# Kernel optimization log

Measured on AMD Instinct MI355X. Metric: run time of the kernel, lower is better.

Reference implementation:

```python
import jax, jax.numpy as jnp
import numpy as np

N_ENTITIES = 100_000
N_USERS = 50_000
N_HOPS = 3
R0, R1 = 42033, 44630  # hard-coded region slice in the source (2597 regions)
CHANNEL = 128
N_EDGES = 2_000_000
NNZ = 1_000_000
N_REL_ROWS = 25  # n_relations - 1


def setup_inputs() -> dict:
    key = jax.random.key(0)
    ks = jax.random.split(key, 10)
    user_emb = jax.random.normal(ks[0], (N_USERS, CHANNEL), jnp.float32) * 0.1
    entity_emb = jax.random.normal(ks[1], (N_ENTITIES, CHANNEL), jnp.float32) * 0.1
    edge_head = jax.random.randint(ks[2], (N_EDGES,), 0, N_ENTITIES, dtype=jnp.int32)
    edge_tail = jax.random.randint(ks[3], (N_EDGES,), 0, N_ENTITIES, dtype=jnp.int32)
    # edge_type in [1, n_relations-1] because weight is indexed with edge_type - 1
    edge_type = jax.random.randint(ks[4], (N_EDGES,), 1, N_REL_ROWS + 1, dtype=jnp.int32)
    interact_rows = jax.random.randint(ks[5], (NNZ,), 0, N_USERS, dtype=jnp.int32)
    interact_cols = jax.random.randint(ks[6], (NNZ,), 0, N_ENTITIES, dtype=jnp.int32)
    interact_vals = jax.random.uniform(ks[7], (NNZ,), jnp.float32)
    rw = jax.random.uniform(ks[8], (R1 - R0, R1 - R0), jnp.float32)
    region_weight_matrix = rw / jnp.sum(rw, axis=1, keepdims=True)  # row-stochastic like source
    weight = jax.random.normal(ks[9], (N_REL_ROWS, CHANNEL), jnp.float32) * 0.1
    return {
        'user_emb': user_emb,
        'entity_emb': entity_emb,
        'region_weight_matrix': region_weight_matrix,
        'weight': weight,
        'interact_vals': interact_vals,
        'edge_head': edge_head,
        'edge_tail': edge_tail,
        'edge_type': edge_type,
        'interact_rows': interact_rows,
        'interact_cols': interact_cols,
    }


def _l2_normalize(x):
    # matches F.normalize(x, p=2, dim=1, eps=1e-12)
    n = jnp.linalg.norm(x, axis=1, keepdims=True)
    return x / jnp.maximum(n, 1e-12)


def reference(user_emb, entity_emb, region_weight_matrix, weight, interact_vals,
              edge_head, edge_tail, edge_type, interact_rows, interact_cols):
    entity_res, user_res = entity_emb, user_emb
    # scatter_mean denominator (edge structure is fixed across hops)
    deg = jax.ops.segment_sum(jnp.ones_like(edge_head, dtype=entity_emb.dtype),
                              edge_head, num_segments=N_ENTITIES)
    inv_deg = jnp.where(deg > 0, 1.0 / deg, 0.0)[:, None]

    for _ in range(N_HOPS):
        # region aggregate (source uses clone().detach())
        new_ev = jax.lax.stop_gradient(entity_emb)
        region = region_weight_matrix @ new_ev[R0:R1]  # [2597, C]
        new_ev = new_ev.at[R0:R1].set(region)
        entity_emb = entity_emb * 0.8 + new_ev * 0.2
        # KG aggregate: gather, relation-weighted multiply, scatter_mean by head
        rel = weight[edge_type - 1]                 # [E, C]
        neigh = entity_emb[edge_tail] * rel          # [E, C]
        entity_agg = jax.ops.segment_sum(neigh, edge_head, num_segments=N_ENTITIES) * inv_deg
        # user aggregate: sparse mm (COO) -> segment_sum over rows
        user_agg = jax.ops.segment_sum(interact_vals[:, None] * entity_emb[interact_cols],
                                       interact_rows, num_segments=N_USERS)
        # normalize + residual (mess_dropout disabled for deterministic reference)
        entity_emb = _l2_normalize(entity_agg)
        user_emb = _l2_normalize(user_agg)
        entity_res = entity_res + entity_emb
        user_res = user_res + user_emb
    return entity_res, user_res
```

## Files before the change

kernel.cpp:

```cpp
#include <hip/hip_runtime.h>
#include <stdint.h>

#define N_ENT 100000
#define N_USR 50000
#define NREG  2597
#define REG0  42033
#define CHAN  128
#define NEDGE 2000000
#define NNZI  1000000

#define BSPAN 512
#define NB_E  196
#define NB_U  98
#define BCAP  11264
#define SLOT_E 12800
#define SLOT_U 12800
#define TILE  2048
#define EPT   8
#define NWG_E ((NEDGE + TILE - 1) / TILE)
#define NWG_U ((NNZI  + TILE - 1) / TILE)

#define MT16   163
#define MPAD   (MT16 * 16)
#define KSTEPS 82
#define KPAD   (KSTEPS * 32)
#define NKC2   8
#define SPC    ((KSTEPS + NKC2 - 1) / NKC2)

typedef unsigned int uint32;
typedef unsigned short ushort16;
using bf16x8 = __attribute__((ext_vector_type(8))) short;
using f32x4  = __attribute__((ext_vector_type(4))) float;

__device__ __forceinline__ uint32 f2bf(float x) {
  uint32 b = __float_as_uint(x);
  b += 0x7FFFu + ((b >> 16) & 1u);
  return b >> 16;
}
__device__ __forceinline__ float bf_lo(uint32 u) { return __uint_as_float(u << 16); }
__device__ __forceinline__ float bf_hi(uint32 u) { return __uint_as_float(u & 0xFFFF0000u); }


__global__ __launch_bounds__(256) void k_part_e(const int* __restrict__ head,
                                                const int* __restrict__ tail,
                                                const int* __restrict__ type,
                                                int* __restrict__ cur,
                                                uint32* __restrict__ st) {
  __shared__ int lh[NB_E], lb[NB_E];
  int tid = threadIdx.x;
  for (int i = tid; i < NB_E; i += 256) lh[i] = 0;
  __syncthreads();
  int base = blockIdx.x * TILE;
  int bk[EPT], rk[EPT]; uint32 rec[EPT];
#pragma unroll
  for (int j = 0; j < EPT; ++j) {
    int idx = base + j * 256 + tid;
    bk[j] = -1;
    if (idx < NEDGE) {
      int h = head[idx];
      uint32 loc = (uint32)(h & (BSPAN - 1));
      rec[j] = (uint32)tail[idx] | ((uint32)(type[idx] - 1) << 17) | (loc << 22);
      bk[j] = h >> 9;
      rk[j] = atomicAdd(&lh[bk[j]], 1);
    }
  }
  __syncthreads();
  for (int i = tid; i < NB_E; i += 256)
    lb[i] = lh[i] ? atomicAdd(&cur[i], lh[i]) : 0;
  __syncthreads();
#pragma unroll
  for (int j = 0; j < EPT; ++j) {
    if (bk[j] >= 0) {
      int slot = lb[bk[j]] + rk[j];
      if (slot < BCAP) st[(size_t)bk[j] * BCAP + slot] = rec[j];
    }
  }
}

__global__ __launch_bounds__(256) void k_part_u(const int* __restrict__ rows,
                                                const int* __restrict__ cols,
                                                const float* __restrict__ vals,
                                                int* __restrict__ cur,
                                                uint2* __restrict__ st) {
  __shared__ int lh[NB_U], lb[NB_U];
  int tid = threadIdx.x;
  for (int i = tid; i < NB_U; i += 256) lh[i] = 0;
  __syncthreads();
  int base = blockIdx.x * TILE;
  int bk[EPT], rk[EPT]; uint2 rec[EPT];
#pragma unroll
  for (int j = 0; j < EPT; ++j) {
    int idx = base + j * 256 + tid;
    bk[j] = -1;
    if (idx < NNZI) {
      int r = rows[idx];
      uint32 loc = (uint32)(r & (BSPAN - 1));
      rec[j] = make_uint2(__float_as_uint(vals[idx]), (uint32)cols[idx] | (loc << 17));
      bk[j] = r >> 9;
      rk[j] = atomicAdd(&lh[bk[j]], 1);
    }
  }
  __syncthreads();
  for (int i = tid; i < NB_U; i += 256)
    lb[i] = lh[i] ? atomicAdd(&cur[i], lh[i]) : 0;
  __syncthreads();
#pragma unroll
  for (int j = 0; j < EPT; ++j) {
    if (bk[j] >= 0) {
      int slot = lb[bk[j]] + rk[j];
      if (slot < BCAP) st[(size_t)bk[j] * BCAP + slot] = rec[j];
    }
  }
}

__global__ __launch_bounds__(512) void k_place_e(const uint32* __restrict__ st,
                                                 const int* __restrict__ bcnt,
                                                 int2* __restrict__ rp2,
                                                 float* __restrict__ invdeg,
                                                 int* __restrict__ pk) {
  __shared__ int hcnt[BSPAN];
  __shared__ int sx[BSPAN];
  int tid = threadIdx.x;
  int b = blockIdx.x;
  int cnt = bcnt[b]; if (cnt > BCAP) cnt = BCAP;
  int base = b * SLOT_E;
  int h0 = b << 9;
  hcnt[tid] = 0;
  __syncthreads();
  const uint32* bst = st + (size_t)b * BCAP;
  for (int i = tid; i < cnt; i += 512)
    atomicAdd(&hcnt[(bst[i] >> 22) & (BSPAN - 1)], 1);
  __syncthreads();
  int mycnt = hcnt[tid];
  int mypad = (mycnt + 3) & ~3;
  sx[tid] = mypad;
  __syncthreads();
  for (int off = 1; off < 512; off <<= 1) {
    int y = (tid >= off) ? sx[tid - off] : 0;
    __syncthreads();
    sx[tid] += y;
    __syncthreads();
  }
  int start = base + sx[tid] - mypad;
  int gh = h0 + tid;
  if (gh < N_ENT) {
    rp2[gh] = make_int2(start, start + mypad);
    invdeg[gh] = mycnt ? 1.0f / (float)mycnt : 0.0f;
  }
  __syncthreads();
  sx[tid] = start;
  hcnt[tid] = 0;
  __syncthreads();
  for (int i = tid; i < cnt; i += 512) {
    uint32 r = bst[i];
    int loc = (r >> 22) & (BSPAN - 1);
    int rk = atomicAdd(&hcnt[loc], 1);
    pk[sx[loc] + rk] = (int)(r & 0x3FFFFFu);
  }
  for (int j = mycnt; j < mypad; ++j) pk[start + j] = (25 << 17);
}

__global__ __launch_bounds__(512) void k_place_u(const uint2* __restrict__ st,
                                                 const int* __restrict__ bcnt,
                                                 int2* __restrict__ rp2,
                                                 int2* __restrict__ pk) {
  __shared__ int hcnt[BSPAN];
  __shared__ int sx[BSPAN];
  int tid = threadIdx.x;
  int b = blockIdx.x;
  int cnt = bcnt[b]; if (cnt > BCAP) cnt = BCAP;
  int base = b * SLOT_U;
  int h0 = b << 9;
  hcnt[tid] = 0;
  __syncthreads();
  const uint2* bst = st + (size_t)b * BCAP;
  for (int i = tid; i < cnt; i += 512)
    atomicAdd(&hcnt[bst[i].y >> 17], 1);
  __syncthreads();
  int mycnt = hcnt[tid];
  int mypad = (mycnt + 3) & ~3;
  sx[tid] = mypad;
  __syncthreads();
  for (int off = 1; off < 512; off <<= 1) {
    int y = (tid >= off) ? sx[tid - off] : 0;
    __syncthreads();
    sx[tid] += y;
    __syncthreads();
  }
  int start = base + sx[tid] - mypad;
  int gh = h0 + tid;
  if (gh < N_USR) rp2[gh] = make_int2(start, start + mypad);
  __syncthreads();
  sx[tid] = start;
  hcnt[tid] = 0;
  __syncthreads();
  for (int i = tid; i < cnt; i += 512) {
    uint2 r = bst[i];
    int loc = r.y >> 17;
    int rk = atomicAdd(&hcnt[loc], 1);
    pk[sx[loc] + rk] = make_int2((int)(r.y & 0x1FFFFu), (int)r.x);
  }
  for (int j = mycnt; j < mypad; ++j) pk[start + j] = make_int2(0, 0);
}

__global__ void k_wt26(const float* __restrict__ w, float* __restrict__ wt) {
  int i = blockIdx.x * blockDim.x + threadIdx.x;
  if (i < 26 * CHAN) wt[i] = (i < 25 * CHAN) ? w[i] : 0.f;
}

__global__ void k_init_ent(const float* __restrict__ src, uint32* __restrict__ dstB,
                           float* __restrict__ out_e, float* __restrict__ Rf) {
  int i = blockIdx.x * blockDim.x + threadIdx.x;
  if (i >= N_ENT * CHAN / 8) return;
  size_t o = (size_t)i * 8;
  float4 v0 = *(const float4*)(src + o);
  float4 v1 = *(const float4*)(src + o + 4);
  uint4 b;
  b.x = f2bf(v0.x) | (f2bf(v0.y) << 16);
  b.y = f2bf(v0.z) | (f2bf(v0.w) << 16);
  b.z = f2bf(v1.x) | (f2bf(v1.y) << 16);
  b.w = f2bf(v1.z) | (f2bf(v1.w) << 16);
  *(uint4*)(dstB + (size_t)i * 4) = b;
  *(float4*)(out_e + o) = v0;
  *(float4*)(out_e + o + 4) = v1;
  int h = (int)(o >> 7);
  if (h >= REG0 && h < REG0 + NREG) {
    size_t ro = (((size_t)(h - REG0)) << 7) + (o & 127);
    *(float4*)(Rf + ro) = v0;
    *(float4*)(Rf + ro + 4) = v1;
  }
}

__global__ void k_cast_rwb(const float* __restrict__ RW, uint32* __restrict__ RWb) {
  int i = blockIdx.x * blockDim.x + threadIdx.x;
  if (i >= MPAD * (KPAD / 8)) return;
  int r = i / (KPAD / 8);
  int k0 = (i % (KPAD / 8)) * 8;
  uint32 o[4];
  if (r < NREG) {
    const float* s = RW + (size_t)r * NREG;
#pragma unroll
    for (int j = 0; j < 4; ++j) {
      int ka = k0 + 2 * j, kb = ka + 1;
      float va = (ka < NREG) ? s[ka] : 0.f;
      float vb = (kb < NREG) ? s[kb] : 0.f;
      o[j] = f2bf(va) | (f2bf(vb) << 16);
    }
  } else {
    o[0] = o[1] = o[2] = o[3] = 0u;
  }
  *(uint4*)(RWb + (size_t)r * (KPAD / 2) + k0 / 2) = make_uint4(o[0], o[1], o[2], o[3]);
}

__global__ void k_build_rbt(const float* __restrict__ Rf, uint32* __restrict__ RbT) {
  int i = blockIdx.x * blockDim.x + threadIdx.x;
  if (i >= CHAN * (KPAD / 8)) return;
  int c = i / (KPAD / 8);
  int k0 = (i % (KPAD / 8)) * 8;
  uint32 o[4];
#pragma unroll
  for (int j = 0; j < 4; ++j) {
    int ka = k0 + 2 * j, kb = ka + 1;
    float va = (ka < NREG) ? Rf[(size_t)ka * CHAN + c] : 0.f;
    float vb = (kb < NREG) ? Rf[(size_t)kb * CHAN + c] : 0.f;
    o[j] = f2bf(va) | (f2bf(vb) << 16);
  }
  *(uint4*)(RbT + (size_t)c * (KPAD / 2) + k0 / 2) = make_uint4(o[0], o[1], o[2], o[3]);
}

__global__ __launch_bounds__(256) void k_region_mfma(const ushort16* __restrict__ RWb,
                                                     const ushort16* __restrict__ RbT,
                                                     float* __restrict__ Rtmp8) {
  int lane = threadIdx.x & 63;
  int wid  = threadIdx.x >> 6;
  int mt = blockIdx.x % MT16;
  int kc = blockIdx.x / MT16;
  int m0 = mt * 16;
  int rc  = lane & 15;
  int kq  = lane >> 4;

  int s0 = kc * SPC;
  int s1 = s0 + SPC; if (s1 > KSTEPS) s1 = KSTEPS;

  f32x4 acc0 = {0.f, 0.f, 0.f, 0.f};
  f32x4 acc1 = {0.f, 0.f, 0.f, 0.f};

  const ushort16* arow = RWb + (size_t)(m0 + rc) * KPAD;
  const ushort16* b0   = RbT + (size_t)(wid * 32 + rc) * KPAD;
  const ushort16* b1   = b0 + (size_t)16 * KPAD;

  for (int s = s0; s < s1; ++s) {
    int k = s * 32 + kq * 8;
    bf16x8 a  = *(const bf16x8*)(arow + k);
    bf16x8 v0 = *(const bf16x8*)(b0 + k);
    bf16x8 v1 = *(const bf16x8*)(b1 + k);
    acc0 = __builtin_amdgcn_mfma_f32_16x16x32_bf16(a, v0, acc0, 0, 0, 0);
    acc1 = __builtin_amdgcn_mfma_f32_16x16x32_bf16(a, v1, acc1, 0, 0, 0);
  }

  float* dst = Rtmp8 + (size_t)kc * (NREG * CHAN);
  int orow = m0 + kq * 4;
#pragma unroll
  for (int r = 0; r < 4; ++r) {
    int gr = orow + r;
    if (gr < NREG) {
      dst[(size_t)gr * CHAN + wid * 32 + rc]      = acc0[r];
      dst[(size_t)gr * CHAN + wid * 32 + 16 + rc] = acc1[r];
    }
  }
}

__global__ void k_region_apply(float* __restrict__ Rf, const float* __restrict__ Rtmp8,
                               ushort16* __restrict__ curB) {
  int i = blockIdx.x * blockDim.x + threadIdx.x;
  if (i < NREG * CHAN) {
    float t = 0.f;
#pragma unroll
    for (int c = 0; c < NKC2; ++c) t += Rtmp8[(size_t)c * (NREG * CHAN) + i];
    float v = Rf[i] * 0.8f + t * 0.2f;
    Rf[i] = v;
    curB[(size_t)REG0 * CHAN + i] = (ushort16)f2bf(v);
  }
}


__global__ void k_ent_agg(const ushort16* __restrict__ curB, const int2* __restrict__ rp2,
                          const int* __restrict__ pk, const float* __restrict__ Wt,
                          const float* __restrict__ invdeg,
                          uint32* __restrict__ nxtB, float* __restrict__ nxtRf,
                          float* __restrict__ out_e) {
  int gid  = blockIdx.x * blockDim.x + threadIdx.x;
  int wave = gid >> 6;
  int lane = threadIdx.x & 63;
  if (wave >= N_ENT) return;
  int h = wave;
  int2 be = rp2[h];
  int beg = be.x, end = be.y;
  int nch = (end - beg) >> 2;
  int e = lane >> 4;
  int q = lane & 15;

  float acc[8];
#pragma unroll
  for (int k = 0; k < 8; ++k) acc[k] = 0.f;

  int pkv = 0;
  { int idx = beg + lane; if (idx < end) pkv = pk[idx]; }

  uint4  ev0, ev1, ev2;
  float4 wa0, wb0, wa1, wb1, wa2, wb2;

#define E_ISSUE(CN, EV, WA, WB) do {                                        \
    int _cn = (CN);                                                         \
    if (_cn < nch) {                                                        \
      if (_cn && ((_cn & 15) == 0)) {                                       \
        int _idx = beg + _cn * 4 + lane;                                    \
        pkv = (_idx < end) ? pk[_idx] : 0;                                  \
      }                                                                     \
      int _p = __shfl(pkv, ((_cn & 15) << 2) | e, 64);                      \
      int _t = _p & 0x1FFFF;                                                \
      int _r = _p >> 17;                                                    \
      EV = *(const uint4*)((const char*)curB + ((size_t)_t << 8) + (q << 4)); \
      const float* _wr = Wt + ((size_t)_r << 7) + (q << 3);                 \
      WA = *(const float4*)_wr;                                             \
      WB = *(const float4*)(_wr + 4);                                       \
    }                                                                       \
  } while (0)

#define E_CONS(EV, WA, WB) do {            \
    acc[0] += bf_lo(EV.x) * WA.x;          \
    acc[1] += bf_hi(EV.x) * WA.y;          \
    acc[2] += bf_lo(EV.y) * WA.z;          \
    acc[3] += bf_hi(EV.y) * WA.w;          \
    acc[4] += bf_lo(EV.z) * WB.x;          \
    acc[5] += bf_hi(EV.z) * WB.y;          \
    acc[6] += bf_lo(EV.w) * WB.z;          \
    acc[7] += bf_hi(EV.w) * WB.w;          \
  } while (0)

  E_ISSUE(0, ev0, wa0, wb0);
  E_ISSUE(1, ev1, wa1, wb1);
  E_ISSUE(2, ev2, wa2, wb2);
  for (int ci = 0; ci < nch; ci += 3) {
    E_CONS(ev0, wa0, wb0);
    E_ISSUE(ci + 3, ev0, wa0, wb0);
    if (ci + 1 < nch) {
      E_CONS(ev1, wa1, wb1);
      E_ISSUE(ci + 4, ev1, wa1, wb1);
    }
    if (ci + 2 < nch) {
      E_CONS(ev2, wa2, wb2);
      E_ISSUE(ci + 5, ev2, wa2, wb2);
    }
  }
#undef E_ISSUE
#undef E_CONS

#pragma unroll
  for (int k = 0; k < 8; ++k) {
    acc[k] += __shfl_xor(acc[k], 16, 64);
    acc[k] += __shfl_xor(acc[k], 32, 64);
  }
  float s = invdeg[h];
#pragma unroll
  for (int k = 0; k < 8; ++k) acc[k] *= s;
  float ss = 0.f;
#pragma unroll
  for (int k = 0; k < 8; ++k) ss += acc[k] * acc[k];
#pragma unroll
  for (int off = 8; off; off >>= 1) ss += __shfl_xor(ss, off, 64);
  float inv = 1.0f / fmaxf(sqrtf(ss), 1e-12f);
#pragma unroll
  for (int k = 0; k < 8; ++k) acc[k] *= inv;

  if (e == 0) {
    uint4 bpk;
    bpk.x = f2bf(acc[0]) | (f2bf(acc[1]) << 16);
    bpk.y = f2bf(acc[2]) | (f2bf(acc[3]) << 16);
    bpk.z = f2bf(acc[4]) | (f2bf(acc[5]) << 16);
    bpk.w = f2bf(acc[6]) | (f2bf(acc[7]) << 16);
    *(uint4*)((char*)nxtB + ((size_t)h << 8) + (q << 4)) = bpk;
    if (h >= REG0 && h < REG0 + NREG) {
      float* rp = nxtRf + ((size_t)(h - REG0) << 7) + (q << 3);
      *(float4*)rp       = make_float4(acc[0], acc[1], acc[2], acc[3]);
      *(float4*)(rp + 4) = make_float4(acc[4], acc[5], acc[6], acc[7]);
    }
    float* op = out_e + ((size_t)h << 7) + (q << 3);
    float4 o0 = *(const float4*)op;
    float4 o1 = *(const float4*)(op + 4);
    o0.x += acc[0]; o0.y += acc[1]; o0.z += acc[2]; o0.w += acc[3];
    o1.x += acc[4]; o1.y += acc[5]; o1.z += acc[6]; o1.w += acc[7];
    *(float4*)op       = o0;
    *(float4*)(op + 4) = o1;
  }
}

__global__ void k_usr_agg(const ushort16* __restrict__ curB, const int2* __restrict__ rp2,
                          const int2* __restrict__ pk, float* __restrict__ out_u) {
  int gid  = blockIdx.x * blockDim.x + threadIdx.x;
  int wave = gid >> 6;
  int lane = threadIdx.x & 63;
  if (wave >= N_USR) return;
  int u = wave;
  int2 be = rp2[u];
  int beg = be.x, end = be.y;
  int nch = (end - beg) >> 2;
  int e = lane >> 4;
  int q = lane & 15;

  float acc[8];
#pragma unroll
  for (int k = 0; k < 8; ++k) acc[k] = 0.f;

  int2 pkv = make_int2(0, 0);
  { int idx = beg + lane; if (idx < end) pkv = pk[idx]; }

  uint4 ev0, ev1, ev2;
  float v0, v1, v2;

#define U_ISSUE(CN, EV, V) do {                                             \
    int _cn = (CN);                                                         \
    if (_cn < nch) {                                                        \
      if (_cn && ((_cn & 15) == 0)) {                                       \
        int _idx = beg + _cn * 4 + lane;                                    \
        pkv = (_idx < end) ? pk[_idx] : make_int2(0, 0);                    \
      }                                                                     \
      int _sl = ((_cn & 15) << 2) | e;                                      \
      int _c = __shfl(pkv.x, _sl, 64);                                      \
      V = __int_as_float(__shfl(pkv.y, _sl, 64));                           \
      EV = *(const uint4*)((const char*)curB + ((size_t)_c << 8) + (q << 4)); \
    }                                                                       \
  } while (0)

#define U_CONS(EV, V) do {          \
    acc[0] += V * bf_lo(EV.x);      \
    acc[1] += V * bf_hi(EV.x);      \
    acc[2] += V * bf_lo(EV.y);      \
    acc[3] += V * bf_hi(EV.y);      \
    acc[4] += V * bf_lo(EV.z);      \
    acc[5] += V * bf_hi(EV.z);      \
    acc[6] += V * bf_lo(EV.w);      \
    acc[7] += V * bf_hi(EV.w);      \
  } while (0)

  U_ISSUE(0, ev0, v0);
  U_ISSUE(1, ev1, v1);
  U_ISSUE(2, ev2, v2);
  for (int ci = 0; ci < nch; ci += 3) {
    U_CONS(ev0, v0);
    U_ISSUE(ci + 3, ev0, v0);
    if (ci + 1 < nch) {
      U_CONS(ev1, v1);
      U_ISSUE(ci + 4, ev1, v1);
    }
    if (ci + 2 < nch) {
      U_CONS(ev2, v2);
      U_ISSUE(ci + 5, ev2, v2);
    }
  }
#undef U_ISSUE
#undef U_CONS

#pragma unroll
  for (int k = 0; k < 8; ++k) {
    acc[k] += __shfl_xor(acc[k], 16, 64);
    acc[k] += __shfl_xor(acc[k], 32, 64);
  }
  float ss = 0.f;
#pragma unroll
  for (int k = 0; k < 8; ++k) ss += acc[k] * acc[k];
#pragma unroll
  for (int off = 8; off; off >>= 1) ss += __shfl_xor(ss, off, 64);
  float inv = 1.0f / fmaxf(sqrtf(ss), 1e-12f);
#pragma unroll
  for (int k = 0; k < 8; ++k) acc[k] *= inv;

  if (e == 0) {
    float* op = out_u + ((size_t)u << 7) + (q << 3);
    float4 o0 = *(const float4*)op;
    float4 o1 = *(const float4*)(op + 4);
    o0.x += acc[0]; o0.y += acc[1]; o0.z += acc[2]; o0.w += acc[3];
    o1.x += acc[4]; o1.y += acc[5]; o1.z += acc[6]; o1.w += acc[7];
    *(float4*)op       = o0;
    *(float4*)(op + 4) = o1;
  }
}


extern "C" void kernel_launch(void* const* d_in, const int* in_sizes, int n_in,
                              void* d_out, int out_size, void* d_ws, size_t ws_size,
                              hipStream_t stream) {
  const float* user_emb   = (const float*)d_in[0];
  const float* entity_emb = (const float*)d_in[1];
  const float* RW         = (const float*)d_in[2];
  const float* weight     = (const float*)d_in[3];
  const float* ivals      = (const float*)d_in[4];
  const int*   e_head     = (const int*)d_in[5];
  const int*   e_tail     = (const int*)d_in[6];
  const int*   e_type     = (const int*)d_in[7];
  const int*   i_rows     = (const int*)d_in[8];
  const int*   i_cols     = (const int*)d_in[9];

  float* out_e = (float*)d_out;
  float* out_u = (float*)d_out + (size_t)N_ENT * CHAN;

  char* p = (char*)d_ws;
  size_t off = 0;
  auto carve = [&](size_t bytes) -> void* {
    void* r = p + off;
    off += (bytes + 255) & ~(size_t)255;
    return r;
  };
  ushort16* B16a   = (ushort16*)carve((size_t)N_ENT * CHAN * 2);
  ushort16* B16b   = (ushort16*)carve((size_t)N_ENT * CHAN * 2);
  ushort16* RWb    = (ushort16*)carve((size_t)MPAD * KPAD * 2);
  ushort16* RbT    = (ushort16*)carve((size_t)CHAN * KPAD * 2);
  float* Rfa       = (float*)carve((size_t)NREG * CHAN * 4);
  float* Rfb       = (float*)carve((size_t)NREG * CHAN * 4);
  float* inv_deg   = (float*)carve((size_t)N_ENT * 4);
  float* wt26      = (float*)carve((size_t)26 * CHAN * 4);
  int2*  e_rp2     = (int2*)carve((size_t)N_ENT * 8);
  int*   e_packed  = (int*)carve((size_t)NB_E * SLOT_E * 4);
  int2*  u_rp2     = (int2*)carve((size_t)N_USR * 8);
  int2*  u_packed  = (int2*)carve((size_t)NB_U * SLOT_U * 8);
  size_t st_bytes   = (size_t)NB_E * BCAP * 4 > (size_t)NB_U * BCAP * 8
                      ? (size_t)NB_E * BCAP * 4 : (size_t)NB_U * BCAP * 8;
  size_t rtmp_bytes = (size_t)NKC2 * NREG * CHAN * 4;
  char*  shared_rg = (char*)carve(st_bytes > rtmp_bytes ? st_bytes : rtmp_bytes);
  float* Rtmp8     = (float*)shared_rg;
  int*   e_bcur    = (int*)carve((size_t)NB_E * 4);
  int*   u_bcur    = (int*)carve((size_t)NB_U * 4);
  if (off > ws_size) return;

  hipMemsetAsync(e_bcur, 0, (size_t)NB_E * 4, stream);
  k_part_e<<<NWG_E, 256, 0, stream>>>(e_head, e_tail, e_type, e_bcur, (uint32*)shared_rg);
  k_place_e<<<NB_E, 512, 0, stream>>>((const uint32*)shared_rg, e_bcur,
                                      e_rp2, inv_deg, e_packed);

  hipMemsetAsync(u_bcur, 0, (size_t)NB_U * 4, stream);
  k_part_u<<<NWG_U, 256, 0, stream>>>(i_rows, i_cols, ivals, u_bcur, (uint2*)shared_rg);
  k_place_u<<<NB_U, 512, 0, stream>>>((const uint2*)shared_rg, u_bcur,
                                      u_rp2, u_packed);

  k_cast_rwb<<<(MPAD * (KPAD / 8) + 255) / 256, 256, 0, stream>>>(RW, (uint32*)RWb);
  k_wt26<<<(26 * CHAN + 255) / 256, 256, 0, stream>>>(weight, wt26);
  k_init_ent<<<(N_ENT * CHAN / 8 + 255) / 256, 256, 0, stream>>>(
      entity_emb, (uint32*)B16a, out_e, Rfa);
  hipMemcpyAsync(out_u, user_emb, (size_t)N_USR * CHAN * 4, hipMemcpyDeviceToDevice, stream);

  for (int hop = 0; hop < 3; ++hop) {
    ushort16* curB = (hop & 1) ? B16b : B16a;
    ushort16* nxtB = (hop & 1) ? B16a : B16b;
    float*    curR = (hop & 1) ? Rfb : Rfa;
    float*    nxtR = (hop & 1) ? Rfa : Rfb;
    k_build_rbt<<<(CHAN * (KPAD / 8) + 255) / 256, 256, 0, stream>>>(curR, (uint32*)RbT);
    k_region_mfma<<<MT16 * NKC2, 256, 0, stream>>>(RWb, RbT, Rtmp8);
    k_region_apply<<<(NREG * CHAN + 255) / 256, 256, 0, stream>>>(curR, Rtmp8, curB);
    k_ent_agg<<<(N_ENT * 64) / 256, 256, 0, stream>>>(curB, e_rp2, e_packed, wt26,
                                                      inv_deg, (uint32*)nxtB, nxtR, out_e);
    k_usr_agg<<<(N_USR * 64) / 256, 256, 0, stream>>>(curB, u_rp2, u_packed, out_u);
  }
}
```

Measured before the change: 808.6 us.

## Fuse entity and user aggregation into one interleaved kernel launch

Merges the entity and user aggregation kernels into a single launch. Blocks are interleaved so that two of every three blocks handle entities and the third handles users, letting both gathers run concurrently and removing the serialization between them. It also swaps the three-deep software prefetch for a simpler double-buffered prefetch, which lowers register pressure but hides less memory latency. Block-level branching on the group index adds some imbalance between entity and user blocks.

```diff
diff --git a/kernel.cpp b/kernel.cpp
--- a/kernel.cpp
+++ b/kernel.cpp
@@ -26,6 +26,9 @@
 #define KPAD   (KSTEPS * 32)
 #define NKC2   8
 #define SPC    ((KSTEPS + NKC2 - 1) / NKC2)
+
+#define NTRIP  12500
+#define NBLK_AGG (NTRIP * 3)
 
 typedef unsigned int uint32;
 typedef unsigned short ushort16;
@@ -324,205 +327,184 @@
 }
 
 
-__global__ void k_ent_agg(const ushort16* __restrict__ curB, const int2* __restrict__ rp2,
-                          const int* __restrict__ pk, const float* __restrict__ Wt,
-                          const float* __restrict__ invdeg,
-                          uint32* __restrict__ nxtB, float* __restrict__ nxtRf,
-                          float* __restrict__ out_e) {
-  int gid  = blockIdx.x * blockDim.x + threadIdx.x;
-  int wave = gid >> 6;
+__global__ __launch_bounds__(256) void k_agg(
+    const ushort16* __restrict__ curB,
+    const int2* __restrict__ erp2, const int* __restrict__ epk,
+    const float* __restrict__ Wt, const float* __restrict__ invdeg,
+    uint32* __restrict__ nxtB, float* __restrict__ nxtRf, float* __restrict__ out_e,
+    const int2* __restrict__ urp2, const int2* __restrict__ upk,
+    float* __restrict__ out_u) {
+  int bid  = blockIdx.x;
+  int wid  = threadIdx.x >> 6;
   int lane = threadIdx.x & 63;
-  if (wave >= N_ENT) return;
-  int h = wave;
-  int2 be = rp2[h];
-  int beg = be.x, end = be.y;
-  int nch = (end - beg) >> 2;
+  int grp  = bid % 3;
+  int trip = bid / 3;
   int e = lane >> 4;
   int q = lane & 15;
 
-  float acc[8];
-#pragma unroll
-  for (int k = 0; k < 8; ++k) acc[k] = 0.f;
-
-  int pkv = 0;
-  { int idx = beg + lane; if (idx < end) pkv = pk[idx]; }
-
-  uint4  ev0, ev1, ev2;
-  float4 wa0, wb0, wa1, wb1, wa2, wb2;
-
-#define E_ISSUE(CN, EV, WA, WB) do {                                        \
-    int _cn = (CN);                                                         \
-    if (_cn < nch) {                                                        \
-      if (_cn && ((_cn & 15) == 0)) {                                       \
-        int _idx = beg + _cn * 4 + lane;                                    \
-        pkv = (_idx < end) ? pk[_idx] : 0;                                  \
-      }                                                                     \
-      int _p = __shfl(pkv, ((_cn & 15) << 2) | e, 64);                      \
-      int _t = _p & 0x1FFFF;                                                \
-      int _r = _p >> 17;                                                    \
-      EV = *(const uint4*)((const char*)curB + ((size_t)_t << 8) + (q << 4)); \
-      const float* _wr = Wt + ((size_t)_r << 7) + (q << 3);                 \
-      WA = *(const float4*)_wr;                                             \
-      WB = *(const float4*)(_wr + 4);                                       \
-    }                                                                       \
-  } while (0)
-
-#define E_CONS(EV, WA, WB) do {            \
-    acc[0] += bf_lo(EV.x) * WA.x;          \
-    acc[1] += bf_hi(EV.x) * WA.y;          \
-    acc[2] += bf_lo(EV.y) * WA.z;          \
-    acc[3] += bf_hi(EV.y) * WA.w;          \
-    acc[4] += bf_lo(EV.z) * WB.x;          \
-    acc[5] += bf_hi(EV.z) * WB.y;          \
-    acc[6] += bf_lo(EV.w) * WB.z;          \
-    acc[7] += bf_hi(EV.w) * WB.w;          \
-  } while (0)
-
-  E_ISSUE(0, ev0, wa0, wb0);
-  E_ISSUE(1, ev1, wa1, wb1);
-  E_ISSUE(2, ev2, wa2, wb2);
-  for (int ci = 0; ci < nch; ci += 3) {
-    E_CONS(ev0, wa0, wb0);
-    E_ISSUE(ci + 3, ev0, wa0, wb0);
-    if (ci + 1 < nch) {
-      E_CONS(ev1, wa1, wb1);
-      E_ISSUE(ci + 4, ev1, wa1, wb1);
-    }
-    if (ci + 2 < nch) {
-      E_CONS(ev2, wa2, wb2);
-      E_ISSUE(ci + 5, ev2, wa2, wb2);
-    }
-  }
-#undef E_ISSUE
-#undef E_CONS
-
-#pragma unroll
-  for (int k = 0; k < 8; ++k) {
-    acc[k] += __shfl_xor(acc[k], 16, 64);
-    acc[k] += __shfl_xor(acc[k], 32, 64);
-  }
-  float s = invdeg[h];
-#pragma unroll
-  for (int k = 0; k < 8; ++k) acc[k] *= s;
-  float ss = 0.f;
-#pragma unroll
-  for (int k = 0; k < 8; ++k) ss += acc[k] * acc[k];
-#pragma unroll
-  for (int off = 8; off; off >>= 1) ss += __shfl_xor(ss, off, 64);
-  float inv = 1.0f / fmaxf(sqrtf(ss), 1e-12f);
-#pragma unroll
-  for (int k = 0; k < 8; ++k) acc[k] *= inv;
-
-  if (e == 0) {
-    uint4 bpk;
-    bpk.x = f2bf(acc[0]) | (f2bf(acc[1]) << 16);
-    bpk.y = f2bf(acc[2]) | (f2bf(acc[3]) << 16);
-    bpk.z = f2bf(acc[4]) | (f2bf(acc[5]) << 16);
-    bpk.w = f2bf(acc[6]) | (f2bf(acc[7]) << 16);
-    *(uint4*)((char*)nxtB + ((size_t)h << 8) + (q << 4)) = bpk;
-    if (h >= REG0 && h < REG0 + NREG) {
-      float* rp = nxtRf + ((size_t)(h - REG0) << 7) + (q << 3);
-      *(float4*)rp       = make_float4(acc[0], acc[1], acc[2], acc[3]);
-      *(float4*)(rp + 4) = make_float4(acc[4], acc[5], acc[6], acc[7]);
-    }
-    float* op = out_e + ((size_t)h << 7) + (q << 3);
-    float4 o0 = *(const float4*)op;
-    float4 o1 = *(const float4*)(op + 4);
-    o0.x += acc[0]; o0.y += acc[1]; o0.z += acc[2]; o0.w += acc[3];
-    o1.x += acc[4]; o1.y += acc[5]; o1.z += acc[6]; o1.w += acc[7];
-    *(float4*)op       = o0;
-    *(float4*)(op + 4) = o1;
-  }
-}
-
-__global__ void k_usr_agg(const ushort16* __restrict__ curB, const int2* __restrict__ rp2,
-                          const int2* __restrict__ pk, float* __restrict__ out_u) {
-  int gid  = blockIdx.x * blockDim.x + threadIdx.x;
-  int wave = gid >> 6;
-  int lane = threadIdx.x & 63;
-  if (wave >= N_USR) return;
-  int u = wave;
-  int2 be = rp2[u];
-  int beg = be.x, end = be.y;
-  int nch = (end - beg) >> 2;
-  int e = lane >> 4;
-  int q = lane & 15;
-
-  float acc[8];
-#pragma unroll
-  for (int k = 0; k < 8; ++k) acc[k] = 0.f;
-
-  int2 pkv = make_int2(0, 0);
-  { int idx = beg + lane; if (idx < end) pkv = pk[idx]; }
-
-  uint4 ev0, ev1, ev2;
-  float v0, v1, v2;
-
-#define U_ISSUE(CN, EV, V) do {                                             \
-    int _cn = (CN);                                                         \
-    if (_cn < nch) {                                                        \
-      if (_cn && ((_cn & 15) == 0)) {                                       \
-        int _idx = beg + _cn * 4 + lane;                                    \
-        pkv = (_idx < end) ? pk[_idx] : make_int2(0, 0);                    \
-      }                                                                     \
-      int _sl = ((_cn & 15) << 2) | e;                                      \
-      int _c = __shfl(pkv.x, _sl, 64);                                      \
-      V = __int_as_float(__shfl(pkv.y, _sl, 64));                           \
-      EV = *(const uint4*)((const char*)curB + ((size_t)_c << 8) + (q << 4)); \
-    }                                                                       \
-  } while (0)
-
-#define U_CONS(EV, V) do {          \
-    acc[0] += V * bf_lo(EV.x);      \
-    acc[1] += V * bf_hi(EV.x);      \
-    acc[2] += V * bf_lo(EV.y);      \
-    acc[3] += V * bf_hi(EV.y);      \
-    acc[4] += V * bf_lo(EV.z);      \
-    acc[5] += V * bf_hi(EV.z);      \
-    acc[6] += V * bf_lo(EV.w);      \
-    acc[7] += V * bf_hi(EV.w);      \
-  } while (0)
-
-  U_ISSUE(0, ev0, v0);
-  U_ISSUE(1, ev1, v1);
-  U_ISSUE(2, ev2, v2);
-  for (int ci = 0; ci < nch; ci += 3) {
-    U_CONS(ev0, v0);
-    U_ISSUE(ci + 3, ev0, v0);
-    if (ci + 1 < nch) {
-      U_CONS(ev1, v1);
-      U_ISSUE(ci + 4, ev1, v1);
-    }
-    if (ci + 2 < nch) {
-      U_CONS(ev2, v2);
-      U_ISSUE(ci + 5, ev2, v2);
-    }
-  }
-#undef U_ISSUE
-#undef U_CONS
-
-#pragma unroll
-  for (int k = 0; k < 8; ++k) {
-    acc[k] += __shfl_xor(acc[k], 16, 64);
-    acc[k] += __shfl_xor(acc[k], 32, 64);
-  }
-  float ss = 0.f;
-#pragma unroll
-  for (int k = 0; k < 8; ++k) ss += acc[k] * acc[k];
-#pragma unroll
-  for (int off = 8; off; off >>= 1) ss += __shfl_xor(ss, off, 64);
-  float inv = 1.0f / fmaxf(sqrtf(ss), 1e-12f);
-#pragma unroll
-  for (int k = 0; k < 8; ++k) acc[k] *= inv;
-
-  if (e == 0) {
-    float* op = out_u + ((size_t)u << 7) + (q << 3);
-    float4 o0 = *(const float4*)op;
-    float4 o1 = *(const float4*)(op + 4);
-    o0.x += acc[0]; o0.y += acc[1]; o0.z += acc[2]; o0.w += acc[3];
-    o1.x += acc[4]; o1.y += acc[5]; o1.z += acc[6]; o1.w += acc[7];
-    *(float4*)op       = o0;
-    *(float4*)(op + 4) = o1;
+  if (grp < 2) {
+    int h = trip * 8 + grp * 4 + wid;
+    int2 be = erp2[h];
+    int beg = be.x, end = be.y;
+    int nch = (end - beg) >> 2;
+
+    float acc[8];
+#pragma unroll
+    for (int k = 0; k < 8; ++k) acc[k] = 0.f;
+
+    int pkv = 0;
+    { int idx = beg + lane; if (idx < end) pkv = epk[idx]; }
+
+    uint4  evA = make_uint4(0, 0, 0, 0);
+    float4 waA = make_float4(0.f, 0.f, 0.f, 0.f);
+    float4 wbA = make_float4(0.f, 0.f, 0.f, 0.f);
+
+    if (nch > 0) {
+      int p = __shfl(pkv, e, 64);
+      int t = p & 0x1FFFF;
+      int r = p >> 17;
+      evA = *(const uint4*)((const char*)curB + ((size_t)t << 8) + (q << 4));
+      const float* wr = Wt + ((size_t)r << 7) + (q << 3);
+      waA = *(const float4*)wr;
+      wbA = *(const float4*)(wr + 4);
+    }
+
+    for (int ci = 0; ci < nch; ++ci) {
+      uint4  evB = make_uint4(0, 0, 0, 0);
+      float4 waB = make_float4(0.f, 0.f, 0.f, 0.f);
+      float4 wbB = make_float4(0.f, 0.f, 0.f, 0.f);
+      int cn = ci + 1;
+      if (cn < nch) {
+        if ((cn & 15) == 0) {
+          int idx = beg + cn * 4 + lane;
+          pkv = (idx < end) ? epk[idx] : 0;
+        }
+        int p = __shfl(pkv, ((cn & 15) << 2) | e, 64);
+        int t = p & 0x1FFFF;
+        int r = p >> 17;
+        evB = *(const uint4*)((const char*)curB + ((size_t)t << 8) + (q << 4));
+        const float* wr = Wt + ((size_t)r << 7) + (q << 3);
+        waB = *(const float4*)wr;
+        wbB = *(const float4*)(wr + 4);
+      }
+      acc[0] += bf_lo(evA.x) * waA.x;
+      acc[1] += bf_hi(evA.x) * waA.y;
+      acc[2] += bf_lo(evA.y) * waA.z;
+      acc[3] += bf_hi(evA.y) * waA.w;
+      acc[4] += bf_lo(evA.z) * wbA.x;
+      acc[5] += bf_hi(evA.z) * wbA.y;
+      acc[6] += bf_lo(evA.w) * wbA.z;
+      acc[7] += bf_hi(evA.w) * wbA.w;
+      evA = evB; waA = waB; wbA = wbB;
+    }
+
+#pragma unroll
+    for (int k = 0; k < 8; ++k) {
+      acc[k] += __shfl_xor(acc[k], 16, 64);
+      acc[k] += __shfl_xor(acc[k], 32, 64);
+    }
+    float s = invdeg[h];
+#pragma unroll
+    for (int k = 0; k < 8; ++k) acc[k] *= s;
+    float ss = 0.f;
+#pragma unroll
+    for (int k = 0; k < 8; ++k) ss += acc[k] * acc[k];
+#pragma unroll
+    for (int off = 8; off; off >>= 1) ss += __shfl_xor(ss, off, 64);
+    float inv = 1.0f / fmaxf(sqrtf(ss), 1e-12f);
+#pragma unroll
+    for (int k = 0; k < 8; ++k) acc[k] *= inv;
+
+    if (e == 0) {
+      uint4 bpk;
+      bpk.x = f2bf(acc[0]) | (f2bf(acc[1]) << 16);
+      bpk.y = f2bf(acc[2]) | (f2bf(acc[3]) << 16);
+      bpk.z = f2bf(acc[4]) | (f2bf(acc[5]) << 16);
+      bpk.w = f2bf(acc[6]) | (f2bf(acc[7]) << 16);
+      *(uint4*)((char*)nxtB + ((size_t)h << 8) + (q << 4)) = bpk;
+      if (h >= REG0 && h < REG0 + NREG) {
+        float* rp = nxtRf + ((size_t)(h - REG0) << 7) + (q << 3);
+        *(float4*)rp       = make_float4(acc[0], acc[1], acc[2], acc[3]);
+        *(float4*)(rp + 4) = make_float4(acc[4], acc[5], acc[6], acc[7]);
+      }
+      float* op = out_e + ((size_t)h << 7) + (q << 3);
+      float4 o0 = *(const float4*)op;
+      float4 o1 = *(const float4*)(op + 4);
+      o0.x += acc[0]; o0.y += acc[1]; o0.z += acc[2]; o0.w += acc[3];
+      o1.x += acc[4]; o1.y += acc[5]; o1.z += acc[6]; o1.w += acc[7];
+      *(float4*)op       = o0;
+      *(float4*)(op + 4) = o1;
+    }
+  } else {
+    int u = trip * 4 + wid;
+    int2 be = urp2[u];
+    int beg = be.x, end = be.y;
+    int nch = (end - beg) >> 2;
+
+    float acc[8];
+#pragma unroll
+    for (int k = 0; k < 8; ++k) acc[k] = 0.f;
+
+    int2 pkv = make_int2(0, 0);
+    { int idx = beg + lane; if (idx < end) pkv = upk[idx]; }
+
+    uint4 evA = make_uint4(0, 0, 0, 0);
+    float vA = 0.f;
+
+    if (nch > 0) {
+      int col = __shfl(pkv.x, e, 64);
+      vA      = __int_as_float(__shfl(pkv.y, e, 64));
+      evA = *(const uint4*)((const char*)curB + ((size_t)col << 8) + (q << 4));
+    }
+
+    for (int ci = 0; ci < nch; ++ci) {
+      uint4 evB = make_uint4(0, 0, 0, 0);
+      float vB = 0.f;
+      int cn = ci + 1;
+      if (cn < nch) {
+        if ((cn & 15) == 0) {
+          int idx = beg + cn * 4 + lane;
+          pkv = (idx < end) ? upk[idx] : make_int2(0, 0);
+        }
+        int sl = ((cn & 15) << 2) | e;
+        int col = __shfl(pkv.x, sl, 64);
+        vB      = __int_as_float(__shfl(pkv.y, sl, 64));
+        evB = *(const uint4*)((const char*)curB + ((size_t)col << 8) + (q << 4));
+      }
+      acc[0] += vA * bf_lo(evA.x);
+      acc[1] += vA * bf_hi(evA.x);
+      acc[2] += vA * bf_lo(evA.y);
+      acc[3] += vA * bf_hi(evA.y);
+      acc[4] += vA * bf_lo(evA.z);
+      acc[5] += vA * bf_hi(evA.z);
+      acc[6] += vA * bf_lo(evA.w);
+      acc[7] += vA * bf_hi(evA.w);
+      evA = evB; vA = vB;
+    }
+
+#pragma unroll
+    for (int k = 0; k < 8; ++k) {
+      acc[k] += __shfl_xor(acc[k], 16, 64);
+      acc[k] += __shfl_xor(acc[k], 32, 64);
+    }
+    float ss = 0.f;
+#pragma unroll
+    for (int k = 0; k < 8; ++k) ss += acc[k] * acc[k];
+#pragma unroll
+    for (int off = 8; off; off >>= 1) ss += __shfl_xor(ss, off, 64);
+    float inv = 1.0f / fmaxf(sqrtf(ss), 1e-12f);
+#pragma unroll
+    for (int k = 0; k < 8; ++k) acc[k] *= inv;
+
+    if (e == 0) {
+      float* op = out_u + ((size_t)u << 7) + (q << 3);
+      float4 o0 = *(const float4*)op;
+      float4 o1 = *(const float4*)(op + 4);
+      o0.x += acc[0]; o0.y += acc[1]; o0.z += acc[2]; o0.w += acc[3];
+      o1.x += acc[4]; o1.y += acc[5]; o1.z += acc[6]; o1.w += acc[7];
+      *(float4*)op       = o0;
+      *(float4*)(op + 4) = o1;
+    }
   }
 }
 
@@ -596,8 +578,8 @@
     k_build_rbt<<<(CHAN * (KPAD / 8) + 255) / 256, 256, 0, stream>>>(curR, (uint32*)RbT);
     k_region_mfma<<<MT16 * NKC2, 256, 0, stream>>>(RWb, RbT, Rtmp8);
     k_region_apply<<<(NREG * CHAN + 255) / 256, 256, 0, stream>>>(curR, Rtmp8, curB);
-    k_ent_agg<<<(N_ENT * 64) / 256, 256, 0, stream>>>(curB, e_rp2, e_packed, wt26,
-                                                      inv_deg, (uint32*)nxtB, nxtR, out_e);
-    k_usr_agg<<<(N_USR * 64) / 256, 256, 0, stream>>>(curB, u_rp2, u_packed, out_u);
-  }
-}
+    k_agg<<<NBLK_AGG, 256, 0, stream>>>(curB, e_rp2, e_packed, wt26, inv_deg,
+                                        (uint32*)nxtB, nxtR, out_e,
+                                        u_rp2, u_packed, out_u);
+  }
+}
```

Result: faster. 759.5 us (-6.1%).
